# Optimization experiments

Hardware: AMD Instinct MI355X
Metric: run time of the kernel (lower is better)

## Reference

```python
import jax, jax.numpy as jnp
import numpy as np

N_NODES = 100000
N_EDGES = 1600000
IN_CH = 256
HID_CH = 128


def setup_inputs() -> dict:
    key = jax.random.key(0)
    k1, k2, k3 = jax.random.split(key, 3)
    x = jax.random.normal(k1, (N_NODES, IN_CH), dtype=jnp.float32)
    edge_index = jax.random.randint(k2, (2, N_EDGES), 0, N_NODES, dtype=jnp.int64)
    # Glorot-style init for the GCN linear weight [in, out]
    W = jax.random.normal(k3, (IN_CH, HID_CH), dtype=jnp.float32) / np.sqrt(IN_CH)
    bias = jnp.zeros((HID_CH,), dtype=jnp.float32)
    # PReLU default init 0.25, per-channel
    alpha = jnp.full((HID_CH,), 0.25, dtype=jnp.float32)
    return {"x": x, "edge_index": edge_index, "W": W, "bias": bias, "alpha": alpha}


def reference(x, edge_index, W, bias, alpha):
    # GCNConv (PyG defaults): add self loops, symmetric degree norm,
    # linear transform then scatter-add aggregation, then per-channel PReLU.
    N = x.shape[0]
    self_loops = jnp.arange(N, dtype=edge_index.dtype)
    row = jnp.concatenate([edge_index[0], self_loops])  # source j
    col = jnp.concatenate([edge_index[1], self_loops])  # target i
    # degree of destination nodes (edge_weight = 1)
    deg = jax.ops.segment_sum(jnp.ones_like(col, dtype=x.dtype), col, num_segments=N)
    dinv = jnp.where(deg > 0, jax.lax.rsqrt(deg), jnp.zeros_like(deg))
    norm = dinv[row] * dinv[col]  # [E+N]
    h = x @ W  # [N, hid] dense transform first (GCNConv order)
    msgs = h[row] * norm[:, None]  # gather + scale, [E+N, hid]
    agg = jax.ops.segment_sum(msgs, col, num_segments=N) + bias  # scatter-add
    # PReLU with per-channel alpha
    return jnp.where(agg > 0, agg, alpha * agg)
```

## Files before the change

### kernel.cpp

```cpp
#include <hip/hip_runtime.h>

#define N_NODES 100000
#define N_EDGES 1600000
#define IN_CH 256
#define HID_CH 128

#define NBUCK 196
#define NBLKC 400
#define EPB   4000
#define SCAN2_LEN (NBUCK * NBLKC)
#define SCAN2_BLOCKS ((SCAN2_LEN + 255) / 256)

typedef __attribute__((ext_vector_type(8))) short short8;
typedef __attribute__((ext_vector_type(4))) float floatx4;

static __device__ __forceinline__ unsigned short f2bf(float f) {
    unsigned int u = __float_as_uint(f);
    u += 0x7fffu + ((u >> 16) & 1u);
    return (unsigned short)(u >> 16);
}

static __device__ __forceinline__ unsigned cvt_pk_bf16(float lo, float hi) {
    unsigned r;
    asm("v_cvt_pk_bf16_f32 %0, %1, %2" : "=v"(r) : "v"(lo), "v"(hi));
    return r;
}


__global__ void hist_kernel(const int* __restrict__ dst, int* __restrict__ histT) {
    __shared__ int h[NBUCK];
    int tid = threadIdx.x, blk = blockIdx.x;
    for (int b = tid; b < NBUCK; b += 256) h[b] = 0;
    __syncthreads();
    int base = blk * EPB;
    for (int e = base + tid; e < base + EPB; e += 256)
        atomicAdd(&h[dst[e] >> 9], 1);
    __syncthreads();
    for (int b = tid; b < NBUCK; b += 256) histT[b * NBLKC + blk] = h[b];
}

__global__ void gscanA_kernel(int* __restrict__ data, int* __restrict__ partials) {
    __shared__ int ss[256];
    int tid = threadIdx.x;
    int i = blockIdx.x * 256 + tid;
    int v = (i < SCAN2_LEN) ? data[i] : 0;
    ss[tid] = v;
    __syncthreads();
    for (int off = 1; off < 256; off <<= 1) {
        int t = (tid >= off) ? ss[tid - off] : 0;
        __syncthreads();
        ss[tid] += t;
        __syncthreads();
    }
    if (i < SCAN2_LEN) data[i] = ss[tid] - v;
    if (tid == 255) partials[blockIdx.x] = ss[255];
}

__global__ void gscanB_kernel(int* __restrict__ partials) {
    __shared__ int ss[512];
    int tid = threadIdx.x;
    int v = (tid < SCAN2_BLOCKS) ? partials[tid] : 0;
    ss[tid] = v;
    __syncthreads();
    for (int off = 1; off < 512; off <<= 1) {
        int t = (tid >= off) ? ss[tid - off] : 0;
        __syncthreads();
        ss[tid] += t;
        __syncthreads();
    }
    if (tid < SCAN2_BLOCKS) partials[tid] = ss[tid] - v;
}

static __device__ __forceinline__ int offs_at(const int* __restrict__ offs,
                                              const int* __restrict__ partials, int i) {
    return offs[i] + partials[i >> 8];
}

__global__ void scatter_coarse_kernel(const int* __restrict__ ei,
                                      const int* __restrict__ offs,
                                      const int* __restrict__ partials,
                                      unsigned* __restrict__ bucketed) {
    __shared__ int cur[NBUCK];
    int tid = threadIdx.x, blk = blockIdx.x;
    for (int b = tid; b < NBUCK; b += 256)
        cur[b] = offs_at(offs, partials, b * NBLKC + blk);
    __syncthreads();
    int base = blk * EPB;
    for (int e = base + tid; e < base + EPB; e += 256) {
        int src = ei[e];
        int dst = ei[N_EDGES + e];
        int b = dst >> 9;
        int pos = atomicAdd(&cur[b], 1);
        bucketed[pos] = ((unsigned)src << 9) | (unsigned)(dst & 511);
    }
}

__global__ void fine_kernel(const unsigned* __restrict__ bucketed,
                            const int* __restrict__ offs,
                            const int* __restrict__ partials,
                            int* __restrict__ sorted,
                            int* __restrict__ row_start,
                            float* __restrict__ dinv) {
    __shared__ int bins[512];
    __shared__ int scanbuf[512];
    int b = blockIdx.x, tid = threadIdx.x;
    int bs = offs_at(offs, partials, b * NBLKC);
    int be = (b < NBUCK - 1) ? offs_at(offs, partials, (b + 1) * NBLKC) : N_EDGES;

    bins[tid] = 0;
    __syncthreads();
    for (int k = bs + tid; k < be; k += 512)
        atomicAdd(&bins[bucketed[k] & 511u], 1);
    __syncthreads();

    int c = bins[tid];
    scanbuf[tid] = c;
    __syncthreads();
    for (int off = 1; off < 512; off <<= 1) {
        int t = (tid >= off) ? scanbuf[tid - off] : 0;
        __syncthreads();
        scanbuf[tid] += t;
        __syncthreads();
    }
    int excl = scanbuf[tid] - c;

    int node = b * 512 + tid;
    if (node <= N_NODES) row_start[node] = bs + excl;
    if (node < N_NODES) dinv[node] = rsqrtf((float)(c + 1));

    bins[tid] = bs + excl;
    __syncthreads();
    for (int k = bs + tid; k < be; k += 512) {
        unsigned p = bucketed[k];
        int pos = atomicAdd(&bins[p & 511u], 1);
        sorted[pos] = (int)(p >> 9);
    }
}


__global__ void wt_kernel(const float* __restrict__ W, unsigned short* __restrict__ Wt) {
    int i = blockIdx.x * blockDim.x + threadIdx.x;
    if (i >= IN_CH * HID_CH) return;
    int k = i >> 7;
    int c = i & 127;
    Wt[c * IN_CH + k] = f2bf(W[i]);
}


__launch_bounds__(512)
__global__ void gemm_mfma_kernel(const float* __restrict__ x,
                                 const unsigned short* __restrict__ Wt,
                                 const float* __restrict__ dinv,
                                 unsigned short* __restrict__ hp) {
    __shared__ unsigned short Bs[IN_CH * HID_CH];

    int tid = threadIdx.x;

    {
        const uint4* src = (const uint4*)Wt;
#pragma unroll
        for (int i = 0; i < 8; ++i) {
            int j = i * 512 + tid;
            unsigned lb = (unsigned)j * 16u;
            unsigned c7 = (lb >> 9) & 7u;
            unsigned db = lb ^ (c7 << 4);
            *(uint4*)((char*)Bs + db) = src[j];
        }
    }
    __syncthreads();

    int wave = tid >> 6;
    int lane = tid & 63;
    int row0 = blockIdx.x * 256 + wave * 32;
    if (row0 >= N_NODES) return;

    int m = lane & 15;
    int q = lane >> 4;

    floatx4 acc[2][8];
#pragma unroll
    for (int i = 0; i < 2; ++i)
#pragma unroll
        for (int t = 0; t < 8; ++t) acc[i][t] = (floatx4){0.f, 0.f, 0.f, 0.f};

    int r0 = row0 + m;        if (r0 >= N_NODES) r0 = N_NODES - 1;
    int r1 = row0 + 16 + m;   if (r1 >= N_NODES) r1 = N_NODES - 1;
    const float* xp0 = &x[(size_t)r0 * IN_CH + q * 8];
    const float* xp1 = &x[(size_t)r1 * IN_CH + q * 8];

    float4 aA[4], aB[4];

#define LOADA(buf, kstep)                                          \
    do {                                                           \
        const float* p0_ = xp0 + (kstep) * 32;                     \
        const float* p1_ = xp1 + (kstep) * 32;                     \
        buf[0] = *(const float4*)(p0_);                            \
        buf[1] = *(const float4*)(p0_ + 4);                        \
        buf[2] = *(const float4*)(p1_);                            \
        buf[3] = *(const float4*)(p1_ + 4);                        \
    } while (0)

#define COMPUTE(buf, kstep)                                                     \
    do {                                                                        \
        union { short8 v; unsigned u[4]; } af0_, af1_;                          \
        af0_.u[0] = cvt_pk_bf16(buf[0].x, buf[0].y);                            \
        af0_.u[1] = cvt_pk_bf16(buf[0].z, buf[0].w);                            \
        af0_.u[2] = cvt_pk_bf16(buf[1].x, buf[1].y);                            \
        af0_.u[3] = cvt_pk_bf16(buf[1].z, buf[1].w);                            \
        af1_.u[0] = cvt_pk_bf16(buf[2].x, buf[2].y);                            \
        af1_.u[1] = cvt_pk_bf16(buf[2].z, buf[2].w);                            \
        af1_.u[2] = cvt_pk_bf16(buf[3].x, buf[3].y);                            \
        af1_.u[3] = cvt_pk_bf16(buf[3].z, buf[3].w);                            \
        int kb_ = ((kstep) * 32 + q * 8) * 2;                                   \
        _Pragma("unroll")                                                       \
        for (int t = 0; t < 8; ++t) {                                           \
            int c_ = t * 16 + m;                                                \
            unsigned db_ = (unsigned)(c_ * 512 + kb_) ^ ((unsigned)(c_ & 7) << 4); \
            short8 bf_ = *(const short8*)((const char*)Bs + db_);               \
            acc[0][t] = __builtin_amdgcn_mfma_f32_16x16x32_bf16(af0_.v, bf_, acc[0][t], 0, 0, 0); \
            acc[1][t] = __builtin_amdgcn_mfma_f32_16x16x32_bf16(af1_.v, bf_, acc[1][t], 0, 0, 0); \
        }                                                                       \
    } while (0)

    LOADA(aA, 0);
#pragma unroll 1
    for (int ks = 0; ks < 8; ks += 2) {
        LOADA(aB, ks + 1);
        COMPUTE(aA, ks);
        if (ks < 6) LOADA(aA, ks + 2);
        COMPUTE(aB, ks + 1);
    }

#undef LOADA
#undef COMPUTE

#pragma unroll
    for (int tile = 0; tile < 2; ++tile) {
#pragma unroll
        for (int reg = 0; reg < 4; ++reg) {
            int grow = row0 + tile * 16 + q * 4 + reg;
            if (grow < N_NODES) {
                float di = dinv[grow];
                unsigned short* op = &hp[(size_t)grow * HID_CH + m];
#pragma unroll
                for (int tp = 0; tp < 4; ++tp) {
                    unsigned d = cvt_pk_bf16(acc[tile][2 * tp][reg] * di,
                                             acc[tile][2 * tp + 1][reg] * di);
                    op[(2 * tp) * 16]     = (unsigned short)(d & 0xffffu);
                    op[(2 * tp + 1) * 16] = (unsigned short)(d >> 16);
                }
            }
        }
    }
}


static __device__ __forceinline__ void acc_bf16x8(float* acc, uint4 u, float w) {
    acc[0] += w * __uint_as_float(u.x << 16);
    acc[1] += w * __uint_as_float(u.x & 0xffff0000u);
    acc[2] += w * __uint_as_float(u.y << 16);
    acc[3] += w * __uint_as_float(u.y & 0xffff0000u);
    acc[4] += w * __uint_as_float(u.z << 16);
    acc[5] += w * __uint_as_float(u.z & 0xffff0000u);
    acc[6] += w * __uint_as_float(u.w << 16);
    acc[7] += w * __uint_as_float(u.w & 0xffff0000u);
}

__launch_bounds__(256)
__global__ void gather_finalize_kernel(const int* __restrict__ row_start,
                                       const int* __restrict__ sorted,
                                       const float* __restrict__ dinv,
                                       const unsigned short* __restrict__ hp,
                                       const float* __restrict__ bias,
                                       const float* __restrict__ alpha,
                                       float* __restrict__ out) {
    int node = (blockIdx.x * blockDim.x + threadIdx.x) >> 6;
    int lane = threadIdx.x & 63;
    if (node >= N_NODES) return;

    int beg = row_start[node];
    int end = row_start[node + 1];
    int part = lane >> 4;
    int ch = (lane & 15) * 8;

    float di = dinv[node];
    uint4 us = *(const uint4*)&hp[(size_t)node * HID_CH + ch];
    float4 bvv0 = *(const float4*)&bias[ch];
    float4 bvv1 = *(const float4*)&bias[ch + 4];
    float4 avv0 = *(const float4*)&alpha[ch];
    float4 avv1 = *(const float4*)&alpha[ch + 4];

    float acc[8];
#pragma unroll
    for (int i = 0; i < 8; ++i) acc[i] = 0.f;

    int e1 = end - 1;
    int k = beg + part;
    if (k < end) {
        int k1 = k + 4, k2 = k + 8, k3 = k + 12;
        int s0 = sorted[k];
        int s1 = sorted[k1 < end ? k1 : e1];
        int s2 = sorted[k2 < end ? k2 : e1];
        int s3 = sorted[k3 < end ? k3 : e1];
        float w1 = k1 < end ? 1.f : 0.f;
        float w2 = k2 < end ? 1.f : 0.f;
        float w3 = k3 < end ? 1.f : 0.f;
        while (true) {
            uint4 u0 = *(const uint4*)&hp[(size_t)s0 * HID_CH + ch];
            uint4 u1 = *(const uint4*)&hp[(size_t)s1 * HID_CH + ch];
            uint4 u2 = *(const uint4*)&hp[(size_t)s2 * HID_CH + ch];
            uint4 u3 = *(const uint4*)&hp[(size_t)s3 * HID_CH + ch];
            float cw1 = w1, cw2 = w2, cw3 = w3;
            int kn = k + 16;
            bool more = kn < end;
            if (more) {
                int n1 = kn + 4, n2 = kn + 8, n3 = kn + 12;
                s0 = sorted[kn];
                s1 = sorted[n1 < end ? n1 : e1];
                s2 = sorted[n2 < end ? n2 : e1];
                s3 = sorted[n3 < end ? n3 : e1];
                w1 = n1 < end ? 1.f : 0.f;
                w2 = n2 < end ? 1.f : 0.f;
                w3 = n3 < end ? 1.f : 0.f;
                k = kn;
            }
            acc_bf16x8(acc, u0, 1.f);
            acc_bf16x8(acc, u1, cw1);
            acc_bf16x8(acc, u2, cw2);
            acc_bf16x8(acc, u3, cw3);
            if (!more) break;
        }
    }

#pragma unroll
    for (int i = 0; i < 8; ++i) {
        acc[i] += __shfl_xor(acc[i], 16);
        acc[i] += __shfl_xor(acc[i], 32);
    }

    if (part == 0) {
        float sf[8];
        sf[0] = __uint_as_float(us.x << 16);
        sf[1] = __uint_as_float(us.x & 0xffff0000u);
        sf[2] = __uint_as_float(us.y << 16);
        sf[3] = __uint_as_float(us.y & 0xffff0000u);
        sf[4] = __uint_as_float(us.z << 16);
        sf[5] = __uint_as_float(us.z & 0xffff0000u);
        sf[6] = __uint_as_float(us.w << 16);
        sf[7] = __uint_as_float(us.w & 0xffff0000u);

        float bv[8] = {bvv0.x, bvv0.y, bvv0.z, bvv0.w, bvv1.x, bvv1.y, bvv1.z, bvv1.w};
        float av[8] = {avv0.x, avv0.y, avv0.z, avv0.w, avv1.x, avv1.y, avv1.z, avv1.w};

        float r[8];
#pragma unroll
        for (int i = 0; i < 8; ++i) {
            float v = di * (acc[i] + sf[i]) + bv[i];
            r[i] = v > 0.f ? v : av[i] * v;
        }
        float4 o0 = make_float4(r[0], r[1], r[2], r[3]);
        float4 o1 = make_float4(r[4], r[5], r[6], r[7]);
        *(float4*)&out[(size_t)node * HID_CH + ch] = o0;
        *(float4*)&out[(size_t)node * HID_CH + ch + 4] = o1;
    }
}


extern "C" void kernel_launch(void* const* d_in, const int* in_sizes, int n_in,
                              void* d_out, int out_size, void* d_ws, size_t ws_size,
                              hipStream_t stream) {
    const float* x     = (const float*)d_in[0];
    const int*   ei    = (const int*)d_in[1];
    const float* W     = (const float*)d_in[2];
    const float* bias  = (const float*)d_in[3];
    const float* alpha = (const float*)d_in[4];
    float* out = (float*)d_out;

    char* p = (char*)d_ws;
    auto align512 = [](size_t v) { return (v + 511) / 512 * 512; };
    unsigned short* hp = (unsigned short*)p; p += align512((size_t)N_NODES * HID_CH * 2);
    unsigned short* Wt = (unsigned short*)p; p += align512((size_t)IN_CH * HID_CH * 2);
    float* dinv    = (float*)p; p += align512((size_t)N_NODES * 4);
    int* row_start = (int*)p;   p += align512((size_t)(N_NODES + 1) * 4);
    int* histT     = (int*)p;   p += align512((size_t)SCAN2_LEN * 4);
    int* partials  = (int*)p;   p += align512(512 * 4);
    unsigned* bucketed = (unsigned*)p; p += align512((size_t)N_EDGES * 4);
    int* sorted    = (int*)p;   p += align512((size_t)N_EDGES * 4);

    hist_kernel<<<NBLKC, 256, 0, stream>>>(ei + N_EDGES, histT);
    gscanA_kernel<<<SCAN2_BLOCKS, 256, 0, stream>>>(histT, partials);
    gscanB_kernel<<<1, 512, 0, stream>>>(partials);
    scatter_coarse_kernel<<<NBLKC, 256, 0, stream>>>(ei, histT, partials, bucketed);
    fine_kernel<<<NBUCK, 512, 0, stream>>>(bucketed, histT, partials, sorted, row_start, dinv);

    wt_kernel<<<(IN_CH * HID_CH + 255) / 256, 256, 0, stream>>>(W, Wt);

    gemm_mfma_kernel<<<(N_NODES + 255) / 256, 512, 0, stream>>>(x, Wt, dinv, hp);

    long long gthreads = (long long)N_NODES * 64;
    gather_finalize_kernel<<<(int)((gthreads + 255) / 256), 256, 0, stream>>>(
        row_start, sorted, dinv, hp, bias, alpha, out);
}
```

Before: 299.3 us.

## Fold weight transpose into histogram kernel, shrink GEMM tiles, simplify gather loop

```diff
diff --git a/kernel.cpp b/kernel.cpp
--- a/kernel.cpp
+++ b/kernel.cpp
@@ -27,9 +27,18 @@
 }
 
 
-__global__ void hist_kernel(const int* __restrict__ dst, int* __restrict__ histT) {
+__global__ void hist_kernel(const int* __restrict__ dst, int* __restrict__ histT,
+                            const float* __restrict__ W, unsigned short* __restrict__ Wt) {
     __shared__ int h[NBUCK];
     int tid = threadIdx.x, blk = blockIdx.x;
+    if (blk == NBLKC) {
+        for (int i = tid; i < IN_CH * HID_CH; i += 256) {
+            int k = i >> 7;
+            int c = i & 127;
+            Wt[c * IN_CH + k] = f2bf(W[i]);
+        }
+        return;
+    }
     for (int b = tid; b < NBUCK; b += 256) h[b] = 0;
     __syncthreads();
     int base = blk * EPB;
@@ -138,16 +147,7 @@
 }
 
 
-__global__ void wt_kernel(const float* __restrict__ W, unsigned short* __restrict__ Wt) {
-    int i = blockIdx.x * blockDim.x + threadIdx.x;
-    if (i >= IN_CH * HID_CH) return;
-    int k = i >> 7;
-    int c = i & 127;
-    Wt[c * IN_CH + k] = f2bf(W[i]);
-}
-
-
-__launch_bounds__(512)
+__launch_bounds__(512, 4)
 __global__ void gemm_mfma_kernel(const float* __restrict__ x,
                                  const unsigned short* __restrict__ Wt,
                                  const float* __restrict__ dinv,
@@ -171,54 +171,42 @@
 
     int wave = tid >> 6;
     int lane = tid & 63;
-    int row0 = blockIdx.x * 256 + wave * 32;
+    int row0 = blockIdx.x * 128 + wave * 16;
     if (row0 >= N_NODES) return;
 
     int m = lane & 15;
     int q = lane >> 4;
 
-    floatx4 acc[2][8];
-#pragma unroll
-    for (int i = 0; i < 2; ++i)
-#pragma unroll
-        for (int t = 0; t < 8; ++t) acc[i][t] = (floatx4){0.f, 0.f, 0.f, 0.f};
+    floatx4 acc[8];
+#pragma unroll
+    for (int t = 0; t < 8; ++t) acc[t] = (floatx4){0.f, 0.f, 0.f, 0.f};
 
     int r0 = row0 + m;        if (r0 >= N_NODES) r0 = N_NODES - 1;
-    int r1 = row0 + 16 + m;   if (r1 >= N_NODES) r1 = N_NODES - 1;
     const float* xp0 = &x[(size_t)r0 * IN_CH + q * 8];
-    const float* xp1 = &x[(size_t)r1 * IN_CH + q * 8];
-
-    float4 aA[4], aB[4];
+
+    float4 aA[2], aB[2];
 
 #define LOADA(buf, kstep)                                          \
     do {                                                           \
         const float* p0_ = xp0 + (kstep) * 32;                     \
-        const float* p1_ = xp1 + (kstep) * 32;                     \
         buf[0] = *(const float4*)(p0_);                            \
         buf[1] = *(const float4*)(p0_ + 4);                        \
-        buf[2] = *(const float4*)(p1_);                            \
-        buf[3] = *(const float4*)(p1_ + 4);                        \
     } while (0)
 
 #define COMPUTE(buf, kstep)                                                     \
     do {                                                                        \
-        union { short8 v; unsigned u[4]; } af0_, af1_;                          \
-        af0_.u[0] = cvt_pk_bf16(buf[0].x, buf[0].y);                            \
-        af0_.u[1] = cvt_pk_bf16(buf[0].z, buf[0].w);                            \
-        af0_.u[2] = cvt_pk_bf16(buf[1].x, buf[1].y);                            \
-        af0_.u[3] = cvt_pk_bf16(buf[1].z, buf[1].w);                            \
-        af1_.u[0] = cvt_pk_bf16(buf[2].x, buf[2].y);                            \
-        af1_.u[1] = cvt_pk_bf16(buf[2].z, buf[2].w);                            \
-        af1_.u[2] = cvt_pk_bf16(buf[3].x, buf[3].y);                            \
-        af1_.u[3] = cvt_pk_bf16(buf[3].z, buf[3].w);                            \
+        union { short8 v; unsigned u[4]; } af_;                                 \
+        af_.u[0] = cvt_pk_bf16(buf[0].x, buf[0].y);                             \
+        af_.u[1] = cvt_pk_bf16(buf[0].z, buf[0].w);                             \
+        af_.u[2] = cvt_pk_bf16(buf[1].x, buf[1].y);                             \
+        af_.u[3] = cvt_pk_bf16(buf[1].z, buf[1].w);                             \
         int kb_ = ((kstep) * 32 + q * 8) * 2;                                   \
         _Pragma("unroll")                                                       \
         for (int t = 0; t < 8; ++t) {                                           \
             int c_ = t * 16 + m;                                                \
             unsigned db_ = (unsigned)(c_ * 512 + kb_) ^ ((unsigned)(c_ & 7) << 4); \
             short8 bf_ = *(const short8*)((const char*)Bs + db_);               \
-            acc[0][t] = __builtin_amdgcn_mfma_f32_16x16x32_bf16(af0_.v, bf_, acc[0][t], 0, 0, 0); \
-            acc[1][t] = __builtin_amdgcn_mfma_f32_16x16x32_bf16(af1_.v, bf_, acc[1][t], 0, 0, 0); \
+            acc[t] = __builtin_amdgcn_mfma_f32_16x16x32_bf16(af_.v, bf_, acc[t], 0, 0, 0); \
         }                                                                       \
     } while (0)
 
@@ -235,20 +223,17 @@
 #undef COMPUTE
 
 #pragma unroll
-    for (int tile = 0; tile < 2; ++tile) {
-#pragma unroll
-        for (int reg = 0; reg < 4; ++reg) {
-            int grow = row0 + tile * 16 + q * 4 + reg;
-            if (grow < N_NODES) {
-                float di = dinv[grow];
-                unsigned short* op = &hp[(size_t)grow * HID_CH + m];
-#pragma unroll
-                for (int tp = 0; tp < 4; ++tp) {
-                    unsigned d = cvt_pk_bf16(acc[tile][2 * tp][reg] * di,
-                                             acc[tile][2 * tp + 1][reg] * di);
-                    op[(2 * tp) * 16]     = (unsigned short)(d & 0xffffu);
-                    op[(2 * tp + 1) * 16] = (unsigned short)(d >> 16);
-                }
+    for (int reg = 0; reg < 4; ++reg) {
+        int grow = row0 + q * 4 + reg;
+        if (grow < N_NODES) {
+            float di = dinv[grow];
+            unsigned short* op = &hp[(size_t)grow * HID_CH + m];
+#pragma unroll
+            for (int tp = 0; tp < 4; ++tp) {
+                unsigned d = cvt_pk_bf16(acc[2 * tp][reg] * di,
+                                         acc[2 * tp + 1][reg] * di);
+                op[(2 * tp) * 16]     = (unsigned short)(d & 0xffffu);
+                op[(2 * tp + 1) * 16] = (unsigned short)(d >> 16);
             }
         }
     }
@@ -294,42 +279,24 @@
 #pragma unroll
     for (int i = 0; i < 8; ++i) acc[i] = 0.f;
 
-    int e1 = end - 1;
-    int k = beg + part;
-    if (k < end) {
+    for (int k = beg + part; k < end; k += 16) {
         int k1 = k + 4, k2 = k + 8, k3 = k + 12;
+        int e1 = end - 1;
         int s0 = sorted[k];
         int s1 = sorted[k1 < end ? k1 : e1];
         int s2 = sorted[k2 < end ? k2 : e1];
         int s3 = sorted[k3 < end ? k3 : e1];
+        uint4 u0 = *(const uint4*)&hp[(size_t)s0 * HID_CH + ch];
+        uint4 u1 = *(const uint4*)&hp[(size_t)s1 * HID_CH + ch];
+        uint4 u2 = *(const uint4*)&hp[(size_t)s2 * HID_CH + ch];
+        uint4 u3 = *(const uint4*)&hp[(size_t)s3 * HID_CH + ch];
         float w1 = k1 < end ? 1.f : 0.f;
         float w2 = k2 < end ? 1.f : 0.f;
         float w3 = k3 < end ? 1.f : 0.f;
-        while (true) {
-            uint4 u0 = *(const uint4*)&hp[(size_t)s0 * HID_CH + ch];
-            uint4 u1 = *(const uint4*)&hp[(size_t)s1 * HID_CH + ch];
-            uint4 u2 = *(const uint4*)&hp[(size_t)s2 * HID_CH + ch];
-            uint4 u3 = *(const uint4*)&hp[(size_t)s3 * HID_CH + ch];
-            float cw1 = w1, cw2 = w2, cw3 = w3;
-            int kn = k + 16;
-            bool more = kn < end;
-            if (more) {
-                int n1 = kn + 4, n2 = kn + 8, n3 = kn + 12;
-                s0 = sorted[kn];
-                s1 = sorted[n1 < end ? n1 : e1];
-                s2 = sorted[n2 < end ? n2 : e1];
-                s3 = sorted[n3 < end ? n3 : e1];
-                w1 = n1 < end ? 1.f : 0.f;
-                w2 = n2 < end ? 1.f : 0.f;
-                w3 = n3 < end ? 1.f : 0.f;
-                k = kn;
-            }
-            acc_bf16x8(acc, u0, 1.f);
-            acc_bf16x8(acc, u1, cw1);
-            acc_bf16x8(acc, u2, cw2);
-            acc_bf16x8(acc, u3, cw3);
-            if (!more) break;
-        }
+        acc_bf16x8(acc, u0, 1.f);
+        acc_bf16x8(acc, u1, w1);
+        acc_bf16x8(acc, u2, w2);
+        acc_bf16x8(acc, u3, w3);
     }
 
 #pragma unroll
@@ -387,15 +354,13 @@
     unsigned* bucketed = (unsigned*)p; p += align512((size_t)N_EDGES * 4);
     int* sorted    = (int*)p;   p += align512((size_t)N_EDGES * 4);
 
-    hist_kernel<<<NBLKC, 256, 0, stream>>>(ei + N_EDGES, histT);
+    hist_kernel<<<NBLKC + 1, 256, 0, stream>>>(ei + N_EDGES, histT, W, Wt);
     gscanA_kernel<<<SCAN2_BLOCKS, 256, 0, stream>>>(histT, partials);
     gscanB_kernel<<<1, 512, 0, stream>>>(partials);
     scatter_coarse_kernel<<<NBLKC, 256, 0, stream>>>(ei, histT, partials, bucketed);
     fine_kernel<<<NBUCK, 512, 0, stream>>>(bucketed, histT, partials, sorted, row_start, dinv);
 
-    wt_kernel<<<(IN_CH * HID_CH + 255) / 256, 256, 0, stream>>>(W, Wt);
-
-    gemm_mfma_kernel<<<(N_NODES + 255) / 256, 512, 0, stream>>>(x, Wt, dinv, hp);
+    gemm_mfma_kernel<<<(N_NODES + 127) / 128, 512, 0, stream>>>(x, Wt, dinv, hp);
 
     long long gthreads = (long long)N_NODES * 64;
     gather_finalize_kernel<<<(int)((gthreads + 255) / 256), 256, 0, stream>>>(
```

New measurement: 333.3 us. 11.4% more time.

## Fold weight transpose into hist kernel, simplify gather loop, tighten GEMM launch bounds

Applied to the files above, without the earlier changes.

```diff
diff --git a/kernel.cpp b/kernel.cpp
--- a/kernel.cpp
+++ b/kernel.cpp
@@ -27,9 +27,18 @@
 }
 
 
-__global__ void hist_kernel(const int* __restrict__ dst, int* __restrict__ histT) {
+__global__ void hist_kernel(const int* __restrict__ dst, int* __restrict__ histT,
+                            const float* __restrict__ W, unsigned short* __restrict__ Wt) {
     __shared__ int h[NBUCK];
     int tid = threadIdx.x, blk = blockIdx.x;
+    if (blk == NBLKC) {
+        for (int i = tid; i < IN_CH * HID_CH; i += 256) {
+            int k = i >> 7;
+            int c = i & 127;
+            Wt[c * IN_CH + k] = f2bf(W[i]);
+        }
+        return;
+    }
     for (int b = tid; b < NBUCK; b += 256) h[b] = 0;
     __syncthreads();
     int base = blk * EPB;
@@ -138,16 +147,7 @@
 }
 
 
-__global__ void wt_kernel(const float* __restrict__ W, unsigned short* __restrict__ Wt) {
-    int i = blockIdx.x * blockDim.x + threadIdx.x;
-    if (i >= IN_CH * HID_CH) return;
-    int k = i >> 7;
-    int c = i & 127;
-    Wt[c * IN_CH + k] = f2bf(W[i]);
-}
-
-
-__launch_bounds__(512)
+__launch_bounds__(512, 4)
 __global__ void gemm_mfma_kernel(const float* __restrict__ x,
                                  const unsigned short* __restrict__ Wt,
                                  const float* __restrict__ dinv,
@@ -294,42 +294,24 @@
 #pragma unroll
     for (int i = 0; i < 8; ++i) acc[i] = 0.f;
 
-    int e1 = end - 1;
-    int k = beg + part;
-    if (k < end) {
+    for (int k = beg + part; k < end; k += 16) {
         int k1 = k + 4, k2 = k + 8, k3 = k + 12;
+        int e1 = end - 1;
         int s0 = sorted[k];
         int s1 = sorted[k1 < end ? k1 : e1];
         int s2 = sorted[k2 < end ? k2 : e1];
         int s3 = sorted[k3 < end ? k3 : e1];
+        uint4 u0 = *(const uint4*)&hp[(size_t)s0 * HID_CH + ch];
+        uint4 u1 = *(const uint4*)&hp[(size_t)s1 * HID_CH + ch];
+        uint4 u2 = *(const uint4*)&hp[(size_t)s2 * HID_CH + ch];
+        uint4 u3 = *(const uint4*)&hp[(size_t)s3 * HID_CH + ch];
         float w1 = k1 < end ? 1.f : 0.f;
         float w2 = k2 < end ? 1.f : 0.f;
         float w3 = k3 < end ? 1.f : 0.f;
-        while (true) {
-            uint4 u0 = *(const uint4*)&hp[(size_t)s0 * HID_CH + ch];
-            uint4 u1 = *(const uint4*)&hp[(size_t)s1 * HID_CH + ch];
-            uint4 u2 = *(const uint4*)&hp[(size_t)s2 * HID_CH + ch];
-            uint4 u3 = *(const uint4*)&hp[(size_t)s3 * HID_CH + ch];
-            float cw1 = w1, cw2 = w2, cw3 = w3;
-            int kn = k + 16;
-            bool more = kn < end;
-            if (more) {
-                int n1 = kn + 4, n2 = kn + 8, n3 = kn + 12;
-                s0 = sorted[kn];
-                s1 = sorted[n1 < end ? n1 : e1];
-                s2 = sorted[n2 < end ? n2 : e1];
-                s3 = sorted[n3 < end ? n3 : e1];
-                w1 = n1 < end ? 1.f : 0.f;
-                w2 = n2 < end ? 1.f : 0.f;
-                w3 = n3 < end ? 1.f : 0.f;
-                k = kn;
-            }
-            acc_bf16x8(acc, u0, 1.f);
-            acc_bf16x8(acc, u1, cw1);
-            acc_bf16x8(acc, u2, cw2);
-            acc_bf16x8(acc, u3, cw3);
-            if (!more) break;
-        }
+        acc_bf16x8(acc, u0, 1.f);
+        acc_bf16x8(acc, u1, w1);
+        acc_bf16x8(acc, u2, w2);
+        acc_bf16x8(acc, u3, w3);
     }
 
 #pragma unroll
@@ -387,14 +369,12 @@
     unsigned* bucketed = (unsigned*)p; p += align512((size_t)N_EDGES * 4);
     int* sorted    = (int*)p;   p += align512((size_t)N_EDGES * 4);
 
-    hist_kernel<<<NBLKC, 256, 0, stream>>>(ei + N_EDGES, histT);
+    hist_kernel<<<NBLKC + 1, 256, 0, stream>>>(ei + N_EDGES, histT, W, Wt);
     gscanA_kernel<<<SCAN2_BLOCKS, 256, 0, stream>>>(histT, partials);
     gscanB_kernel<<<1, 512, 0, stream>>>(partials);
     scatter_coarse_kernel<<<NBLKC, 256, 0, stream>>>(ei, histT, partials, bucketed);
     fine_kernel<<<NBUCK, 512, 0, stream>>>(bucketed, histT, partials, sorted, row_start, dinv);
 
-    wt_kernel<<<(IN_CH * HID_CH + 255) / 256, 256, 0, stream>>>(W, Wt);
-
     gemm_mfma_kernel<<<(N_NODES + 255) / 256, 512, 0, stream>>>(x, Wt, dinv, hp);
 
     long long gthreads = (long long)N_NODES * 64;
```

After: 331.6 us. +10.8%, slower.
